# Kernel optimization log

Hardware: AMD Instinct MI355X
Metric: run time of the kernel (lower is better)

Reference implementation:

```python
import jax, jax.numpy as jnp
import numpy as np

B, C, W, H = 4, 256, 64, 64

def setup_inputs() -> dict:
    key = jax.random.key(0)
    ks = jax.random.split(key, 6)
    return {
        "fm_source": jax.random.normal(ks[0], (B, C, W, H), dtype=jnp.float32),
        "fm_reference": jax.random.normal(ks[1], (B, C, W, H), dtype=jnp.float32),
        "w_lambda": jax.random.normal(ks[2], (1, C, 1, 1), dtype=jnp.float32) * 0.05,
        "b_lambda": jax.random.normal(ks[3], (1,), dtype=jnp.float32) * 0.05,
        "w_beta": jax.random.normal(ks[4], (1, C, 1, 1), dtype=jnp.float32) * 0.05,
        "b_beta": jax.random.normal(ks[5], (1,), dtype=jnp.float32) * 0.05,
    }

def reference(fm_source, fm_reference, w_lambda, b_lambda, w_beta, b_beta):
    b, c, w, h = fm_reference.shape
    n = w * h
    # 1x1 convs on the reference feature map -> per-pixel scalars, flattened to [B, N]
    wl = w_lambda.reshape(c)
    wb = w_beta.reshape(c)
    ref_flat = fm_reference.reshape(b, c, n)   # [B, C, N]
    src_flat = fm_source.reshape(b, c, n)      # [B, C, N]
    old_lambda = jnp.einsum("bcn,c->bn", ref_flat, wl) + b_lambda[0]  # [B, N]
    old_beta = jnp.einsum("bcn,c->bn", ref_flat, wb) + b_beta[0]      # [B, N]
    # energy[b, i, j] = <src pixel i, ref pixel j> over channels
    energy = jnp.einsum("bci,bcj->bij", src_flat, ref_flat)  # [B, N, N]
    attention = jax.nn.softmax(energy, axis=-1)              # softmax over ref pixels j
    # new_lambda[b, i] = sum_j old_lambda[b, j] * attention[b, i, j]
    new_lambda = jnp.einsum("bj,bij->bi", old_lambda, attention).reshape(b, 1, w, h)
    new_beta = jnp.einsum("bj,bij->bi", old_beta, attention).reshape(b, 1, w, h)
    # broadcast modulation over the 256 channels
    return new_lambda * fm_source + new_beta
```

## Files before the change

### kernel.cpp

```cpp
#include <hip/hip_runtime.h>


#define B_ 4
#define C_ 256
#define N_ 4096
#define LOG2E 1.44269504f
#define SHIFT2 86.5617f
#define JSLICE 8
#define BN_ (B_ * N_)
#define NT_ 16

typedef _Float16 half_t;
typedef _Float16 v8h  __attribute__((ext_vector_type(8)));
typedef _Float16 v4h  __attribute__((ext_vector_type(4)));
typedef float    v16f __attribute__((ext_vector_type(16)));

#define GLDS16(g, l) __builtin_amdgcn_global_load_lds(                         \
    (const __attribute__((address_space(1))) void*)(g),                        \
    (__attribute__((address_space(3))) void*)(l), 16, 0, 0)

__global__ void k_prep(const float* __restrict__ src,
                       const float* __restrict__ ref,
                       const float* __restrict__ wl, const float* __restrict__ bl,
                       const float* __restrict__ wb, const float* __restrict__ bb,
                       half_t* __restrict__ s16, half_t* __restrict__ r16,
                       float* __restrict__ oldL, float* __restrict__ oldB) {
    if (blockIdx.z == 8) {
        int b  = blockIdx.y;
        int n0 = blockIdx.x * 64;
        int nl = threadIdx.x & 63;
        int cq = threadIdx.x >> 6;
        const float* p = ref + ((size_t)b * C_ + cq * 64) * N_ + n0 + nl;
        float aL = 0.f, aB = 0.f;
#pragma unroll 8
        for (int c = 0; c < 64; c++) {
            float v = p[(size_t)c * N_];
            aL += v * wl[cq * 64 + c];
            aB += v * wb[cq * 64 + c];
        }
        __shared__ float red[8][64];
        red[cq][nl]     = aL;
        red[4 + cq][nl] = aB;
        __syncthreads();
        if (threadIdx.x < 64) {
            int t = threadIdx.x;
            oldL[(size_t)b * N_ + n0 + t] =
                red[0][t] + red[1][t] + red[2][t] + red[3][t] + bl[0];
        } else if (threadIdx.x < 128) {
            int t = threadIdx.x - 64;
            oldB[(size_t)b * N_ + n0 + t] =
                red[4][t] + red[5][t] + red[6][t] + red[7][t] + bb[0];
        }
        return;
    }
    __shared__ float tile[64][65];
    int z  = blockIdx.z;
    int b  = z & 3;
    const float* in  = (z < B_) ? src : ref;
    half_t*      out = (z < B_) ? s16 : r16;
    float scale      = (z < B_) ? LOG2E : 1.0f;
    int c0 = blockIdx.y * 64;
    int n0 = blockIdx.x * 64;
    int tx = threadIdx.x & 15, ty = threadIdx.x >> 4;
#pragma unroll
    for (int q = 0; q < 4; q++) {
        int c = ty + q * 16;
        float4 v = *(const float4*)(in + ((size_t)b * C_ + c0 + c) * N_ + n0 + tx * 4);
        tile[c][tx * 4 + 0] = v.x;
        tile[c][tx * 4 + 1] = v.y;
        tile[c][tx * 4 + 2] = v.z;
        tile[c][tx * 4 + 3] = v.w;
    }
    __syncthreads();
    int r   = threadIdx.x & 31;
    int lhi = (threadIdx.x >> 5) & 1;
    int wv  = threadIdx.x >> 6;
#pragma unroll
    for (int nt = 0; nt < 2; nt++) {
        int nl = nt * 32 + r;
        v8h o;
#pragma unroll
        for (int e = 0; e < 8; e++)
            o[e] = (half_t)(tile[wv * 16 + lhi * 8 + e][nl] * scale);
        size_t tj = (size_t)(n0 >> 5) + nt;
        size_t kb = (size_t)(c0 >> 4) + wv;
        *(v8h*)(out + ((((size_t)b * 128 + tj) * 16 + kb) * 64 + (threadIdx.x & 63)) * 8) = o;
    }
}

__global__ __launch_bounds__(512, 2) void k_flash(
        const half_t* __restrict__ sT, const half_t* __restrict__ rT,
        const float* __restrict__ oldL, const float* __restrict__ oldB,
        float* __restrict__ part ) {
    __shared__ half_t lds[2][8192];
    int bid    = blockIdx.x;
    int b      = bid & 3;
    int jslice = (bid >> 2) & (JSLICE - 1);
    int iblock = bid >> 5;
    int tid    = threadIdx.x;
    int wv     = tid >> 6;
    int lane   = tid & 63;
    int l31    = lane & 31, lhi = lane >> 5;
    int ti     = iblock * 8 + wv;
    int i0     = ti * 32;
    int j0     = jslice * (N_ / JSLICE);
    int tj0    = j0 >> 5;

    const half_t* aP = sT + (((size_t)b * 128 + ti) * 16) * 512 + (size_t)lane * 8;
    v8h a[16];
#pragma unroll
    for (int kb = 0; kb < 16; kb++) a[kb] = *(const v8h*)(aP + (size_t)kb * 512);

    const half_t* bBase = rT + (((size_t)b * 128 + tj0) * 16) * 512;
    const float*  oLp = oldL + (size_t)b * N_ + j0 + l31;
    const float*  oBp = oldB + (size_t)b * N_ + j0 + l31;

    float sp[16], sl[16], sb[16];
#pragma unroll
    for (int r = 0; r < 16; r++) { sp[r] = 0.f; sl[r] = 0.f; sb[r] = 0.f; }

#pragma unroll
    for (int q = 0; q < 2; q++) {
        int chunk = q * 8 + wv;
        GLDS16(bBase + (size_t)chunk * 512 + (size_t)lane * 8,
               &lds[0][(size_t)chunk * 512]);
    }

    for (int jt = 0; jt < NT_; jt++) {
        __syncthreads();
        if (jt + 1 < NT_) {
            const half_t* g = bBase + (size_t)(jt + 1) * 8192;
#pragma unroll
            for (int q = 0; q < 2; q++) {
                int chunk = q * 8 + wv;
                GLDS16(g + (size_t)chunk * 512 + (size_t)lane * 8,
                       &lds[(jt + 1) & 1][(size_t)chunk * 512]);
            }
        }
        const half_t* bt = lds[jt & 1] + (size_t)lane * 8;
        v16f acc0, acc1;
#pragma unroll
        for (int r = 0; r < 16; r++) { acc0[r] = -SHIFT2; acc1[r] = 0.f; }
#pragma unroll
        for (int kb = 0; kb < 8; kb++) {
            acc0 = __builtin_amdgcn_mfma_f32_32x32x16_f16(
                a[kb],     *(const v8h*)(bt + (size_t)kb * 512),       acc0, 0, 0, 0);
            acc1 = __builtin_amdgcn_mfma_f32_32x32x16_f16(
                a[kb + 8], *(const v8h*)(bt + (size_t)(kb + 8) * 512), acc1, 0, 0, 0);
        }
        float lam = oLp[jt * 32], bet = oBp[jt * 32];
#pragma unroll
        for (int r = 0; r < 16; r++) {
            float p = __builtin_amdgcn_exp2f(acc0[r] + acc1[r]);
            sp[r] += p;
            sl[r] += p * lam;
            sb[r] += p * bet;
        }
    }

    float* pSP = part + ((size_t)jslice * 3 + 0) * BN_;
    float* pSL = part + ((size_t)jslice * 3 + 1) * BN_;
    float* pSB = part + ((size_t)jslice * 3 + 2) * BN_;
#pragma unroll
    for (int r = 0; r < 16; r++) {
        float tp = sp[r], tl = sl[r], tb = sb[r];
#pragma unroll
        for (int m = 1; m <= 16; m <<= 1) {
            tp += __shfl_xor(tp, m, 64);
            tl += __shfl_xor(tl, m, 64);
            tb += __shfl_xor(tb, m, 64);
        }
        if (l31 == 0) {
            int row = (r & 3) + 8 * (r >> 2) + 4 * lhi;
            size_t ig = (size_t)b * N_ + i0 + row;
            pSP[ig] = tp; pSL[ig] = tl; pSB[ig] = tb;
        }
    }
}

__global__ void k_post(const float* __restrict__ src,
                       const float* __restrict__ part,
                       float* __restrict__ out) {
    int b  = blockIdx.x;
    int n0 = blockIdx.y * 1024;
    int c0 = blockIdx.z * 16;
    int t  = threadIdx.x;
    size_t bn = (size_t)b * N_ + n0 + t * 4;
    float4 sp = {0.f, 0.f, 0.f, 0.f}, sl = sp, sb = sp;
#pragma unroll
    for (int s = 0; s < JSLICE; s++) {
        float4 p0 = *(const float4*)(part + ((size_t)s * 3 + 0) * BN_ + bn);
        float4 p1 = *(const float4*)(part + ((size_t)s * 3 + 1) * BN_ + bn);
        float4 p2 = *(const float4*)(part + ((size_t)s * 3 + 2) * BN_ + bn);
        sp.x += p0.x; sp.y += p0.y; sp.z += p0.z; sp.w += p0.w;
        sl.x += p1.x; sl.y += p1.y; sl.z += p1.z; sl.w += p1.w;
        sb.x += p2.x; sb.y += p2.y; sb.z += p2.z; sb.w += p2.w;
    }
    float4 L, T;
    L.x = sl.x / sp.x; L.y = sl.y / sp.y; L.z = sl.z / sp.z; L.w = sl.w / sp.w;
    T.x = sb.x / sp.x; T.y = sb.y / sp.y; T.z = sb.z / sp.z; T.w = sb.w / sp.w;
    const float* sp0 = src + ((size_t)b * C_ + c0) * N_ + n0 + t * 4;
    float*       op0 = out + ((size_t)b * C_ + c0) * N_ + n0 + t * 4;
#pragma unroll 4
    for (int c = 0; c < 16; c++) {
        float4 v = *(const float4*)(sp0 + (size_t)c * N_);
        float4 o;
        o.x = L.x * v.x + T.x;
        o.y = L.y * v.y + T.y;
        o.z = L.z * v.z + T.z;
        o.w = L.w * v.w + T.w;
        *(float4*)(op0 + (size_t)c * N_) = o;
    }
}

extern "C" void kernel_launch(void* const* d_in, const int* in_sizes, int n_in,
                              void* d_out, int out_size, void* d_ws, size_t ws_size,
                              hipStream_t stream) {
    const float* src = (const float*)d_in[0];
    const float* ref = (const float*)d_in[1];
    const float* wl  = (const float*)d_in[2];
    const float* bl  = (const float*)d_in[3];
    const float* wb  = (const float*)d_in[4];
    const float* bb  = (const float*)d_in[5];
    float* out = (float*)d_out;

    float* oldL = (float*)d_ws;
    float* oldB = oldL + BN_;
    float* part = oldB + BN_;
    size_t needF  = ((size_t)2 + 3 * JSLICE) * BN_ * sizeof(float);
    size_t need16 = (size_t)2 * B_ * N_ * C_ * sizeof(half_t);
    half_t* s16;
    if (ws_size >= needF + need16) s16 = (half_t*)((char*)d_ws + needF);
    else                           s16 = (half_t*)d_out;
    half_t* r16 = s16 + (size_t)B_ * N_ * C_;

    k_prep<<<dim3(N_ / 64, C_ / 64, 9), 256, 0, stream>>>(
        src, ref, wl, bl, wb, bb, s16, r16, oldL, oldB);
    k_flash<<<512, 512, 0, stream>>>(s16, r16, oldL, oldB, part);
    k_post<<<dim3(B_, N_ / 1024, C_ / 16), 256, 0, stream>>>(src, part, out);
}
```

Baseline: 146.8 us.

## Triple-buffer flash K tiles, stage oldL/oldB in LDS, split combine from post

The flash kernel moves from double to triple buffering of the reference tiles. It prefetches two tiles ahead and replaces the per-iteration __syncthreads with explicit vmcnt waits plus a raw barrier, aiming to hide global-to-LDS latency. The per-column lambda/beta values are loaded once into shared memory instead of from global memory on every tile. A new k_comb kernel reduces the slice partials into new lambda/beta once, so k_post no longer re-reads all partials for every channel block, and k_post now uses smaller channel groups. The costs are an extra kernel launch, more LDS per block, and reliance on hand-placed wait counts.

```diff
diff --git a/kernel.cpp b/kernel.cpp
--- a/kernel.cpp
+++ b/kernel.cpp
@@ -9,10 +9,10 @@
 #define JSLICE 8
 #define BN_ (B_ * N_)
 #define NT_ 16
+#define NBUF 3
 
 typedef _Float16 half_t;
 typedef _Float16 v8h  __attribute__((ext_vector_type(8)));
-typedef _Float16 v4h  __attribute__((ext_vector_type(4)));
 typedef float    v16f __attribute__((ext_vector_type(16)));
 
 #define GLDS16(g, l) __builtin_amdgcn_global_load_lds(                         \
@@ -92,7 +92,8 @@
         const half_t* __restrict__ sT, const half_t* __restrict__ rT,
         const float* __restrict__ oldL, const float* __restrict__ oldB,
         float* __restrict__ part ) {
-    __shared__ half_t lds[2][8192];
+    __shared__ half_t lds[NBUF][8192];
+    __shared__ float oL[512], oB[512];
     int bid    = blockIdx.x;
     int b      = bid & 3;
     int jslice = (bid >> 2) & (JSLICE - 1);
@@ -111,33 +112,43 @@
 #pragma unroll
     for (int kb = 0; kb < 16; kb++) a[kb] = *(const v8h*)(aP + (size_t)kb * 512);
 
+    oL[tid] = oldL[(size_t)b * N_ + j0 + tid];
+    oB[tid] = oldB[(size_t)b * N_ + j0 + tid];
+
     const half_t* bBase = rT + (((size_t)b * 128 + tj0) * 16) * 512;
-    const float*  oLp = oldL + (size_t)b * N_ + j0 + l31;
-    const float*  oBp = oldB + (size_t)b * N_ + j0 + l31;
 
     float sp[16], sl[16], sb[16];
 #pragma unroll
     for (int r = 0; r < 16; r++) { sp[r] = 0.f; sl[r] = 0.f; sb[r] = 0.f; }
 
 #pragma unroll
-    for (int q = 0; q < 2; q++) {
-        int chunk = q * 8 + wv;
-        GLDS16(bBase + (size_t)chunk * 512 + (size_t)lane * 8,
-               &lds[0][(size_t)chunk * 512]);
-    }
+    for (int t = 0; t < 2; t++)
+#pragma unroll
+        for (int q = 0; q < 2; q++) {
+            int chunk = q * 8 + wv;
+            GLDS16(bBase + (size_t)t * 8192 + (size_t)chunk * 512 + (size_t)lane * 8,
+                   &lds[t][(size_t)chunk * 512]);
+        }
+    __syncthreads();
 
     for (int jt = 0; jt < NT_; jt++) {
-        __syncthreads();
-        if (jt + 1 < NT_) {
-            const half_t* g = bBase + (size_t)(jt + 1) * 8192;
+        if (jt < NT_ - 1) asm volatile("s_waitcnt vmcnt(2)" ::: "memory");
+        else              asm volatile("s_waitcnt vmcnt(0)" ::: "memory");
+        __builtin_amdgcn_s_barrier();
+        __builtin_amdgcn_sched_barrier(0);
+        if (jt + 2 < NT_) {
+            const half_t* g = bBase + (size_t)(jt + 2) * 8192;
+            half_t* dst = &lds[(jt + 2) % NBUF][0];
 #pragma unroll
             for (int q = 0; q < 2; q++) {
                 int chunk = q * 8 + wv;
                 GLDS16(g + (size_t)chunk * 512 + (size_t)lane * 8,
-                       &lds[(jt + 1) & 1][(size_t)chunk * 512]);
+                       dst + (size_t)chunk * 512);
             }
         }
-        const half_t* bt = lds[jt & 1] + (size_t)lane * 8;
+        const half_t* bt = &lds[jt % NBUF][0] + (size_t)lane * 8;
+        float lam = oL[jt * 32 + l31];
+        float bet = oB[jt * 32 + l31];
         v16f acc0, acc1;
 #pragma unroll
         for (int r = 0; r < 16; r++) { acc0[r] = -SHIFT2; acc1[r] = 0.f; }
@@ -148,7 +159,6 @@
             acc1 = __builtin_amdgcn_mfma_f32_32x32x16_f16(
                 a[kb + 8], *(const v8h*)(bt + (size_t)(kb + 8) * 512), acc1, 0, 0, 0);
         }
-        float lam = oLp[jt * 32], bet = oBp[jt * 32];
 #pragma unroll
         for (int r = 0; r < 16; r++) {
             float p = __builtin_amdgcn_exp2f(acc0[r] + acc1[r]);
@@ -178,31 +188,34 @@
     }
 }
 
+__global__ void k_comb(const float* __restrict__ part,
+                       float* __restrict__ newLT ) {
+    int g = blockIdx.x * 256 + threadIdx.x;
+    float sp = 0.f, sl = 0.f, sb = 0.f;
+#pragma unroll
+    for (int s = 0; s < JSLICE; s++) {
+        sp += part[((size_t)s * 3 + 0) * BN_ + g];
+        sl += part[((size_t)s * 3 + 1) * BN_ + g];
+        sb += part[((size_t)s * 3 + 2) * BN_ + g];
+    }
+    newLT[g]       = sl / sp;
+    newLT[BN_ + g] = sb / sp;
+}
+
 __global__ void k_post(const float* __restrict__ src,
-                       const float* __restrict__ part,
+                       const float* __restrict__ newLT,
                        float* __restrict__ out) {
     int b  = blockIdx.x;
     int n0 = blockIdx.y * 1024;
-    int c0 = blockIdx.z * 16;
+    int c0 = blockIdx.z * 4;
     int t  = threadIdx.x;
     size_t bn = (size_t)b * N_ + n0 + t * 4;
-    float4 sp = {0.f, 0.f, 0.f, 0.f}, sl = sp, sb = sp;
-#pragma unroll
-    for (int s = 0; s < JSLICE; s++) {
-        float4 p0 = *(const float4*)(part + ((size_t)s * 3 + 0) * BN_ + bn);
-        float4 p1 = *(const float4*)(part + ((size_t)s * 3 + 1) * BN_ + bn);
-        float4 p2 = *(const float4*)(part + ((size_t)s * 3 + 2) * BN_ + bn);
-        sp.x += p0.x; sp.y += p0.y; sp.z += p0.z; sp.w += p0.w;
-        sl.x += p1.x; sl.y += p1.y; sl.z += p1.z; sl.w += p1.w;
-        sb.x += p2.x; sb.y += p2.y; sb.z += p2.z; sb.w += p2.w;
-    }
-    float4 L, T;
-    L.x = sl.x / sp.x; L.y = sl.y / sp.y; L.z = sl.z / sp.z; L.w = sl.w / sp.w;
-    T.x = sb.x / sp.x; T.y = sb.y / sp.y; T.z = sb.z / sp.z; T.w = sb.w / sp.w;
+    float4 L = *(const float4*)(newLT + bn);
+    float4 T = *(const float4*)(newLT + BN_ + bn);
     const float* sp0 = src + ((size_t)b * C_ + c0) * N_ + n0 + t * 4;
     float*       op0 = out + ((size_t)b * C_ + c0) * N_ + n0 + t * 4;
-#pragma unroll 4
-    for (int c = 0; c < 16; c++) {
+#pragma unroll
+    for (int c = 0; c < 4; c++) {
         float4 v = *(const float4*)(sp0 + (size_t)c * N_);
         float4 o;
         o.x = L.x * v.x + T.x;
@@ -224,10 +237,11 @@
     const float* bb  = (const float*)d_in[5];
     float* out = (float*)d_out;
 
-    float* oldL = (float*)d_ws;
-    float* oldB = oldL + BN_;
-    float* part = oldB + BN_;
-    size_t needF  = ((size_t)2 + 3 * JSLICE) * BN_ * sizeof(float);
+    float* oldL  = (float*)d_ws;
+    float* oldB  = oldL + BN_;
+    float* part  = oldB + BN_;
+    float* newLT = part + (size_t)3 * JSLICE * BN_;
+    size_t needF  = ((size_t)2 + 3 * JSLICE + 2) * BN_ * sizeof(float);
     size_t need16 = (size_t)2 * B_ * N_ * C_ * sizeof(half_t);
     half_t* s16;
     if (ws_size >= needF + need16) s16 = (half_t*)((char*)d_ws + needF);
@@ -237,5 +251,6 @@
     k_prep<<<dim3(N_ / 64, C_ / 64, 9), 256, 0, stream>>>(
         src, ref, wl, bl, wb, bb, s16, r16, oldL, oldB);
     k_flash<<<512, 512, 0, stream>>>(s16, r16, oldL, oldB, part);
-    k_post<<<dim3(B_, N_ / 1024, C_ / 16), 256, 0, stream>>>(src, part, out);
-}
+    k_comb<<<BN_ / 256, 256, 0, stream>>>(part, newLT);
+    k_post<<<dim3(B_, N_ / 1024, C_ / 4), 256, 0, stream>>>(src, newLT, out);
+}
```

New measurement: 146.7 us. About the same (-0.0%).
